# Kernel optimization log

Hardware: AMD Instinct MI355X
Metric: run time of the kernel (lower is better)

The kernel has to match this reference:

```python
import jax, jax.numpy as jnp
import numpy as np

SFREQ = 200.0
PATCH = 60
STRIDE = 30           # patch_size * (1 - overlap)
NPERSEG = min(PATCH // 2, 32)   # = 30
STEP = NPERSEG // 2   # scipy welch default noverlap = nperseg//2
NSEG = (PATCH - NPERSEG) // STEP + 1
NF = NPERSEG // 2 + 1
_w = 0.5 * (1.0 - np.cos(2.0 * np.pi * np.arange(NPERSEG) / NPERSEG))  # periodic hann (scipy default)
HANN = jnp.asarray(_w, jnp.float32)
WIN_NORM = float(SFREQ * np.sum(_w ** 2))  # density scaling
_f = np.arange(NF) * SFREQ / NPERSEG
FREQS = jnp.asarray(_f, jnp.float32)
BANDS = jnp.asarray(np.stack([((_f >= lo) & (_f <= hi)).astype(np.float32)
                              for lo, hi in [(1, 4), (4, 8), (8, 13), (13, 30), (30, 99)]]), jnp.float32)
ONESIDED = jnp.asarray(np.concatenate([[1.0], 2.0 * np.ones(NF - 2), [1.0]]), jnp.float32)


def layer_norm(v, g, b, eps=1e-5):
    mu = v.mean(-1, keepdims=True)
    var = ((v - mu) ** 2).mean(-1, keepdims=True)
    return (v - mu) * jax.lax.rsqrt(var + eps) * g + b


def features(p):
    # p: (B, P, PATCH)
    L = p.shape[-1]
    mx = p.max(-1); mn = p.min(-1); mean = p.mean(-1)
    c = p - mean[..., None]
    m2 = (c ** 2).mean(-1); m3 = (c ** 3).mean(-1); m4 = (c ** 4).mean(-1)
    std = jnp.sqrt(m2)
    peak_loc = jnp.argmax(jnp.abs(p), -1).astype(jnp.float32) / L
    dx = jnp.diff(p, axis=-1)
    zc = jnp.sum(jnp.diff(jnp.sign(p + 1e-10), axis=-1) != 0, axis=-1).astype(jnp.float32) / L
    kurt = m4 / (m2 ** 2) - 3.0   # scipy Fisher, biased
    skew = m3 / (m2 ** 1.5)
    morph = jnp.stack([mx, mn, mx - mn, mean, std, peak_loc,
                       dx.max(-1), dx.min(-1), jnp.abs(dx).mean(-1),
                       zc, (p ** 2).sum(-1), kurt, skew], -1)
    morph = jnp.where(jnp.isfinite(morph), morph, 0.0)
    # Welch PSD (detrend='constant', hann, density, one-sided, mean over segments)
    seg_idx = jnp.arange(NSEG)[:, None] * STEP + jnp.arange(NPERSEG)
    segs = p[..., seg_idx]                             # (B,P,NSEG,NPERSEG)
    segs = (segs - segs.mean(-1, keepdims=True)) * HANN
    X = jnp.fft.rfft(segs, axis=-1)                    # (B,P,NSEG,NF)
    psd = ((X.real ** 2 + X.imag ** 2) / WIN_NORM * ONESIDED).mean(-2)  # (B,P,NF)
    total = psd.sum(-1) + 1e-12
    bandp = jnp.einsum('bpf,kf->bpk', psd, BANDS) / total[..., None]
    peakf = FREQS[jnp.argmax(psd, -1)]
    cs = jnp.cumsum(psd, -1)
    edge = FREQS[jnp.argmax(cs >= 0.95 * total[..., None], -1)]
    pn = psd / total[..., None]
    ent = -jnp.sum(pn * jnp.log2(pn + 1e-12), -1)
    spec = jnp.concatenate([bandp, jnp.stack([peakf, edge, ent, total], -1)], -1)
    spec = jnp.where(jnp.isfinite(spec), spec, 0.0)
    return morph, spec


def setup_inputs() -> dict:
    key = jax.random.key(0)
    ks = jax.random.split(key, 8)
    B, T, E = 1024, 6000, 256
    n_m, n_s = 13, 9
    nf = n_m + n_s
    x = jax.random.normal(ks[0], (B, 1, T), jnp.float32)
    return {
        'x': x,
        'g_m': jnp.ones((n_m,), jnp.float32), 'b_m': jnp.zeros((n_m,), jnp.float32),
        'g_s': jnp.ones((n_s,), jnp.float32), 'b_s': jnp.zeros((n_s,), jnp.float32),
        'W1': jax.random.normal(ks[1], (nf, E // 2), jnp.float32) * 0.05,
        'b1': jnp.zeros((E // 2,), jnp.float32),
        'W2': jax.random.normal(ks[2], (E // 2, E), jnp.float32) * 0.05,
        'b2': jnp.zeros((E,), jnp.float32),
        'g_o': jnp.ones((E,), jnp.float32), 'b_o': jnp.zeros((E,), jnp.float32),
    }


def reference(x, g_m, b_m, g_s, b_s, W1, b1, W2, b2, g_o, b_o):
    B, _, T = x.shape
    n_patches = (T - PATCH) // STRIDE + 1
    idx = jnp.arange(n_patches)[:, None] * STRIDE + jnp.arange(PATCH)
    p = x[:, 0, :][:, idx]                     # (B, n_patches, PATCH)
    morph, spec = features(p)
    combined = jnp.concatenate([layer_norm(morph, g_m, b_m), layer_norm(spec, g_s, b_s)], -1)
    h = jax.nn.gelu(combined @ W1 + b1, approximate=False)  # dropout = identity (eval)
    return layer_norm(h @ W2 + b2, g_o, b_o)   # (B, n_patches, emb_size)
```

## Files before the change

kernel.cpp:

```cpp
#include <hip/hip_runtime.h>
#include <math.h>

#define NPERSEG 30
#define STEPW 15
#define NSEG 3
#define NF 16
#define PATCH 60
#define STRIDE 30
#define NP_ROW 199
#define NBATCH 1024
#define T_LEN 6000
#define NPATCH_TOTAL (NBATCH * NP_ROW)
#define GB 32
#define NBLK_B (NPATCH_TOTAL / GB)

constexpr double TC[30] = {
  1.0,
  0.97814760073380563793,
  0.91354545764260089550,
  0.80901699437494742410,
  0.66913060635885821383,
  0.5,
  0.30901699437494742410,
  0.10452846326765347140,
 -0.10452846326765347140,
 -0.30901699437494742410,
 -0.5,
 -0.66913060635885821383,
 -0.80901699437494742410,
 -0.91354545764260089550,
 -0.97814760073380563793,
 -1.0,
 -0.97814760073380563793,
 -0.91354545764260089550,
 -0.80901699437494742410,
 -0.66913060635885821383,
 -0.5,
 -0.30901699437494742410,
 -0.10452846326765347140,
  0.10452846326765347140,
  0.30901699437494742410,
  0.5,
  0.66913060635885821383,
  0.80901699437494742410,
  0.91354545764260089550,
  0.97814760073380563793,
};
constexpr double TS[30] = {
  0.0,
  0.20791169081775933710,
  0.40673664307580020775,
  0.58778525229247312917,
  0.74314482547739423501,
  0.86602540378443864676,
  0.95105651629515357212,
  0.99452189536827333692,
  0.99452189536827333692,
  0.95105651629515357212,
  0.86602540378443864676,
  0.74314482547739423501,
  0.58778525229247312917,
  0.40673664307580020775,
  0.20791169081775933710,
  0.0,
 -0.20791169081775933710,
 -0.40673664307580020775,
 -0.58778525229247312917,
 -0.74314482547739423501,
 -0.86602540378443864676,
 -0.95105651629515357212,
 -0.99452189536827333692,
 -0.99452189536827333692,
 -0.95105651629515357212,
 -0.86602540378443864676,
 -0.74314482547739423501,
 -0.58778525229247312917,
 -0.40673664307580020775,
 -0.20791169081775933710,
};
constexpr double INV_WN = 1.0 / 2250.0;
constexpr double THIRD  = 1.0 / 3.0;

__device__ __forceinline__ float np_sum30_f32(const float* a) {
    float r[8];
#pragma unroll
    for (int j = 0; j < 8; ++j) r[j] = a[j];
#pragma unroll
    for (int i = 8; i < 24; i += 8)
#pragma unroll
        for (int j = 0; j < 8; ++j) r[j] += a[i + j];
    float res = ((r[0] + r[1]) + (r[2] + r[3])) + ((r[4] + r[5]) + (r[6] + r[7]));
#pragma unroll
    for (int i = 24; i < 30; ++i) res += a[i];
    return res;
}

__device__ __forceinline__ double np_sum16_f64(const double* a) {
    double r[8];
#pragma unroll
    for (int j = 0; j < 8; ++j) r[j] = a[j] + a[8 + j];
    return ((r[0] + r[1]) + (r[2] + r[3])) + ((r[4] + r[5]) + (r[6] + r[7]));
}

__global__ __launch_bounds__(256) void feat_kernel(
    const float* __restrict__ x,
    const float* __restrict__ g_m, const float* __restrict__ b_m,
    const float* __restrict__ g_s, const float* __restrict__ b_s,
    float* __restrict__ out)
{
    __shared__ float xs[T_LEN];

    const int tid = threadIdx.x;
    const int row = blockIdx.x;

    {
        const float4* src = reinterpret_cast<const float4*>(x + (size_t)row * T_LEN);
        float4* dst = reinterpret_cast<float4*>(xs);
        for (int i = tid; i < T_LEN / 4; i += 256) dst[i] = src[i];
    }
    __syncthreads();
    if (tid >= NP_ROW) return;

    const float* pf = xs + tid * STRIDE;
    const int p = row * NP_ROW + tid;
    float* op = out + (size_t)(p >> 5) * (GB * 256) + (size_t)(p & 31) * 22;

    double morph[13];
    {
        const float v0f = pf[0];
        const double v0 = (double)v0f;
        double vmax = v0, vmin = v0, vsum = v0;
        float aval = fabsf(v0f); int amax = 0;
        float sv0 = v0f + 1e-10f;
        int prev = (sv0 > 0.0f) - (sv0 < 0.0f);
        int zc = 0;
        double dmax = 0.0, dmin = 0.0, dabssum = 0.0;
        double vprev = v0;
#pragma unroll
        for (int n = 1; n < PATCH; ++n) {
            const float vf = pf[n];
            const double v = (double)vf;
            vmax = fmax(vmax, v); vmin = fmin(vmin, v); vsum += v;
            const float a = fabsf(vf);
            if (a > aval) { aval = a; amax = n; }
            const float sv = vf + 1e-10f;
            const int sg = (sv > 0.0f) - (sv < 0.0f);
            if (sg != prev) zc++;
            prev = sg;
            const double d = v - vprev;
            if (n == 1) { dmax = d; dmin = d; dabssum = fabs(d); }
            else { dmax = fmax(dmax, d); dmin = fmin(dmin, d); dabssum += fabs(d); }
            vprev = v;
        }
        const double vmean = vsum / 60.0;
        const double dabsmean = dabssum / 59.0;
        const double peak_loc = (double)((float)amax / 60.0f);
        const double zcf = (double)zc / 60.0;

        double s2 = 0.0, s3 = 0.0, s4 = 0.0, ssq = 0.0;
#pragma unroll
        for (int n = 0; n < PATCH; ++n) {
            const double v = (double)pf[n];
            const double c = v - vmean, c2 = c * c;
            s2 += c2; s3 += c2 * c; s4 += c2 * c2;
            ssq += v * v;
        }
        const double m2 = s2 / 60.0, m3 = s3 / 60.0, m4 = s4 / 60.0;
        const double vstd = sqrt(m2);
        const double kurt = m4 / (m2 * m2) - 3.0;
        const double skew = m3 / (m2 * sqrt(m2));

        morph[0] = vmax;  morph[1] = vmin;  morph[2] = vmax - vmin;
        morph[3] = vmean; morph[4] = vstd;  morph[5] = peak_loc;
        morph[6] = dmax;  morph[7] = dmin;  morph[8] = dabsmean;
        morph[9] = zcf;   morph[10] = ssq;  morph[11] = kurt; morph[12] = skew;
#pragma unroll
        for (int i = 0; i < 13; ++i) if (!isfinite(morph[i])) morph[i] = 0.0;
    }
    {
        double mu = 0.0;
#pragma unroll
        for (int i = 0; i < 13; ++i) mu += morph[i];
        mu /= 13.0;
        double var = 0.0;
#pragma unroll
        for (int i = 0; i < 13; ++i) { double d = morph[i] - mu; var += d * d; }
        var /= 13.0;
        const double inv = 1.0 / sqrt(var + 1e-5);
        float fm[13];
#pragma unroll
        for (int i = 0; i < 13; ++i)
            fm[i] = (float)((morph[i] - mu) * inv * (double)g_m[i] + (double)b_m[i]);
#pragma unroll
        for (int i = 0; i < 6; ++i)
            *reinterpret_cast<float2*>(op + 2 * i) = make_float2(fm[2 * i], fm[2 * i + 1]);
        op[12] = fm[12];
    }

    asm volatile("" ::: "memory");

    double psd[NF];
#pragma unroll
    for (int k = 0; k < NF; ++k) psd[k] = 0.0;

#pragma unroll 1
    for (int s = 0; s < NSEG; ++s) {
        float y[NPERSEG];
        {
            float q[NPERSEG];
#pragma unroll
            for (int n = 0; n < NPERSEG; ++n) q[n] = pf[s * STEPW + n];
            const float res = np_sum30_f32(q);
            const float smean = res / 30.0f;
#pragma unroll
            for (int n = 0; n < NPERSEG; ++n) {
                const float hn = (float)(0.5 * (1.0 - TC[n]));
                y[n] = (q[n] - smean) * hn;
            }
        }

        {
            double re[8], im[8];
#pragma unroll
            for (int j = 0; j < 8; ++j) { re[j] = 0.0; im[j] = 0.0; }
#pragma unroll
            for (int m = 0; m < NPERSEG; ++m) {
                const double yd = (double)y[m];
#pragma unroll
                for (int j = 0; j < 8; ++j) {
                    const double tcv = TC[(j * m) % 30];
                    const double tsv = TS[(j * m) % 30];
                    re[j] += yd * tcv;
                    if (tsv != 0.0) im[j] += yd * tsv;
                }
            }
#pragma unroll
            for (int j = 0; j < 8; ++j) {
                double pw = re[j] * re[j] + im[j] * im[j];
                pw *= INV_WN;
                if (j != 0) pw = pw + pw;
                psd[j] += pw;
            }
        }
        {
            double re[8], im[8];
#pragma unroll
            for (int j = 0; j < 8; ++j) { re[j] = 0.0; im[j] = 0.0; }
#pragma unroll
            for (int m = 0; m < NPERSEG; ++m) {
                const double yd = (double)y[m];
#pragma unroll
                for (int j = 0; j < 8; ++j) {
                    const int k = 8 + j;
                    const double tcv = TC[(k * m) % 30];
                    const double tsv = TS[(k * m) % 30];
                    re[j] += yd * tcv;
                    if (tsv != 0.0) im[j] += yd * tsv;
                }
            }
#pragma unroll
            for (int j = 0; j < 8; ++j) {
                double pw = re[j] * re[j] + im[j] * im[j];
                pw *= INV_WN;
                if (j != 7) pw = pw + pw;
                psd[8 + j] += pw;
            }
        }
    }
#pragma unroll
    for (int k = 0; k < NF; ++k) psd[k] = psd[k] * THIRD;

    const double total = np_sum16_f64(psd) + 1e-12;
    const double invt = 1.0 / total;

    const double band1 = psd[1] * invt;
    const double band3 = ((psd[2] + psd[3]) + psd[4]) * invt;
    double b4s = 0.0;
#pragma unroll
    for (int k = 5; k <= 14; ++k) b4s += psd[k];
    const double band4 = b4s * invt;

    int bk = 0; double bpv = psd[0];
#pragma unroll
    for (int k = 1; k < NF; ++k) if (psd[k] > bpv) { bpv = psd[k]; bk = k; }

    const double th = 0.95 * total;
    int ek = 0;
    {
        double acc = 0.0; bool found = false;
#pragma unroll
        for (int k = 0; k < NF; ++k) {
            acc += psd[k];
            if (!found && acc >= th) { ek = k; found = true; }
        }
    }

    double ent = 0.0;
#pragma unroll
    for (int k = 0; k < NF; ++k) {
        const double pn = psd[k] * invt;
        ent -= pn * log2(pn + 1e-12);
    }

    double spec[9];
    spec[0] = 0.0;
    spec[1] = band1;
    spec[2] = 0.0;
    spec[3] = band3;
    spec[4] = band4;
    spec[5] = (double)((float)((double)bk * 200.0 / 30.0));
    spec[6] = (double)((float)((double)ek * 200.0 / 30.0));
    spec[7] = ent;
    spec[8] = total;
#pragma unroll
    for (int i = 0; i < 9; ++i) if (!isfinite(spec[i])) spec[i] = 0.0;

    {
        double mu = 0.0;
#pragma unroll
        for (int i = 0; i < 9; ++i) mu += spec[i];
        mu /= 9.0;
        double var = 0.0;
#pragma unroll
        for (int i = 0; i < 9; ++i) { double d = spec[i] - mu; var += d * d; }
        var /= 9.0;
        const double inv = 1.0 / sqrt(var + 1e-5);
        float fs[9];
#pragma unroll
        for (int i = 0; i < 9; ++i)
            fs[i] = (float)((spec[i] - mu) * inv * (double)g_s[i] + (double)b_s[i]);
        op[13] = fs[0];
#pragma unroll
        for (int i = 0; i < 4; ++i)
            *reinterpret_cast<float2*>(op + 14 + 2 * i) = make_float2(fs[1 + 2 * i], fs[2 + 2 * i]);
    }
}

__global__ __launch_bounds__(256, 4) void mlp_kernel(
    const float* __restrict__ W1, const float* __restrict__ b1,
    const float* __restrict__ W2, const float* __restrict__ b2,
    const float* __restrict__ g_o, const float* __restrict__ b_o,
    float* __restrict__ out)
{
    __shared__ float Fsl[GB * 22];
    __shared__ float Hs[GB][128];

    const int tid = threadIdx.x;
    const size_t base = (size_t)blockIdx.x * (GB * 256);

    if (tid < 176)
        reinterpret_cast<float4*>(Fsl)[tid] =
            *reinterpret_cast<const float4*>(out + base + 4 * (size_t)tid);
    __syncthreads();

    {
        const int hc  = tid & 127;
        const int ppb = tid >> 7;
        float w1c[22];
#pragma unroll
        for (int k = 0; k < 22; ++k) w1c[k] = W1[k * 128 + hc];
        const float b1v = b1[hc];
#pragma unroll
        for (int v = 0; v < 16; ++v) {
            const int pp = ppb + 2 * v;
            float a = b1v;
#pragma unroll
            for (int k = 0; k < 22; ++k) a += Fsl[pp * 22 + k] * w1c[k];
            Hs[pp][hc] = 0.5f * a * (1.0f + erff(a * 0.70710678118654752440f));
        }
    }
    __syncthreads();

    const int lane  = tid & 63;
    const int wv    = tid >> 6;
    const int half  = lane >> 5;
    const int l5    = lane & 31;
    const int ch0   = l5 * 8;
    const int pbase = 8 * wv + 4 * half;

    float4 accA[4], accB[4];
    {
        const float4 b2lo = *reinterpret_cast<const float4*>(b2 + ch0);
        const float4 b2hi = *reinterpret_cast<const float4*>(b2 + ch0 + 4);
#pragma unroll
        for (int pp = 0; pp < 4; ++pp) { accA[pp] = b2lo; accB[pp] = b2hi; }
    }

#pragma unroll 2
    for (int k = 0; k < 128; k += 4) {
        float4 h[4];
#pragma unroll
        for (int pp = 0; pp < 4; ++pp)
            h[pp] = *reinterpret_cast<const float4*>(&Hs[pbase + pp][k]);
        float4 wlo[4], whi[4];
#pragma unroll
        for (int kk = 0; kk < 4; ++kk) {
            wlo[kk] = *reinterpret_cast<const float4*>(&W2[(k + kk) * 256 + ch0]);
            whi[kk] = *reinterpret_cast<const float4*>(&W2[(k + kk) * 256 + ch0 + 4]);
        }
#pragma unroll
        for (int kk = 0; kk < 4; ++kk) {
#pragma unroll
            for (int pp = 0; pp < 4; ++pp) {
                const float hv = (kk == 0) ? h[pp].x : (kk == 1) ? h[pp].y
                               : (kk == 2) ? h[pp].z : h[pp].w;
                accA[pp].x += hv * wlo[kk].x; accA[pp].y += hv * wlo[kk].y;
                accA[pp].z += hv * wlo[kk].z; accA[pp].w += hv * wlo[kk].w;
                accB[pp].x += hv * whi[kk].x; accB[pp].y += hv * whi[kk].y;
                accB[pp].z += hv * whi[kk].z; accB[pp].w += hv * whi[kk].w;
            }
        }
    }

    const float4 golo = *reinterpret_cast<const float4*>(g_o + ch0);
    const float4 gohi = *reinterpret_cast<const float4*>(g_o + ch0 + 4);
    const float4 bolo = *reinterpret_cast<const float4*>(b_o + ch0);
    const float4 bohi = *reinterpret_cast<const float4*>(b_o + ch0 + 4);
#pragma unroll
    for (int pp = 0; pp < 4; ++pp) {
        float s = ((accA[pp].x + accA[pp].y) + (accA[pp].z + accA[pp].w))
                + ((accB[pp].x + accB[pp].y) + (accB[pp].z + accB[pp].w));
        float q = ((accA[pp].x * accA[pp].x + accA[pp].y * accA[pp].y)
                +  (accA[pp].z * accA[pp].z + accA[pp].w * accA[pp].w))
                + ((accB[pp].x * accB[pp].x + accB[pp].y * accB[pp].y)
                +  (accB[pp].z * accB[pp].z + accB[pp].w * accB[pp].w));
        for (int off = 16; off; off >>= 1) {
            s += __shfl_xor(s, off);
            q += __shfl_xor(q, off);
        }
        const float mu  = s * (1.0f / 256.0f);
        const float var = q * (1.0f / 256.0f) - mu * mu;
        const float inv = rsqrtf(var + 1e-5f);
        float4 oA, oB;
        oA.x = (accA[pp].x - mu) * inv * golo.x + bolo.x;
        oA.y = (accA[pp].y - mu) * inv * golo.y + bolo.y;
        oA.z = (accA[pp].z - mu) * inv * golo.z + bolo.z;
        oA.w = (accA[pp].w - mu) * inv * golo.w + bolo.w;
        oB.x = (accB[pp].x - mu) * inv * gohi.x + bohi.x;
        oB.y = (accB[pp].y - mu) * inv * gohi.y + bohi.y;
        oB.z = (accB[pp].z - mu) * inv * gohi.z + bohi.z;
        oB.w = (accB[pp].w - mu) * inv * gohi.w + bohi.w;
        float* orow = out + base + (size_t)(pbase + pp) * 256 + ch0;
        *reinterpret_cast<float4*>(orow)     = oA;
        *reinterpret_cast<float4*>(orow + 4) = oB;
    }
}

extern "C" void kernel_launch(void* const* d_in, const int* in_sizes, int n_in,
                              void* d_out, int out_size, void* d_ws, size_t ws_size,
                              hipStream_t stream) {
    const float* x   = (const float*)d_in[0];
    const float* g_m = (const float*)d_in[1];
    const float* b_m = (const float*)d_in[2];
    const float* g_s = (const float*)d_in[3];
    const float* b_s = (const float*)d_in[4];
    const float* W1  = (const float*)d_in[5];
    const float* b1  = (const float*)d_in[6];
    const float* W2  = (const float*)d_in[7];
    const float* b2  = (const float*)d_in[8];
    const float* g_o = (const float*)d_in[9];
    const float* b_o = (const float*)d_in[10];
    float* out = (float*)d_out;

    feat_kernel<<<NBATCH, 256, 0, stream>>>(x, g_m, b_m, g_s, b_s, out);
    mlp_kernel<<<NBLK_B, 256, 0, stream>>>(W1, b1, W2, b2, g_o, b_o, out);
}
```

Baseline: 481.0 us.

## Fold real-input DFT symmetry and remap MLP second layer to one row per wave

The per-segment DFT now pairs y[m] with y[30-m], using their sum for the cosine terms and their difference for the sine terms. This roughly halves the double-precision multiply-adds in the Welch PSD. The second-layer GEMM in the MLP kernel is remapped so each thread owns 4 output channels across 8 patches, with one full wave covering a 256-wide row and a 64-lane reduction for the layer norm. Launch bounds rise to 8 blocks per CU, which restricts register usage and may cause spilling.

```diff
diff --git a/kernel.cpp b/kernel.cpp
--- a/kernel.cpp
+++ b/kernel.cpp
@@ -218,20 +218,26 @@
                 y[n] = (q[n] - smean) * hn;
             }
         }
+        const double y0d  = (double)y[0];
+        const double y15d = (double)y[15];
 
         {
             double re[8], im[8];
 #pragma unroll
-            for (int j = 0; j < 8; ++j) { re[j] = 0.0; im[j] = 0.0; }
-#pragma unroll
-            for (int m = 0; m < NPERSEG; ++m) {
-                const double yd = (double)y[m];
+            for (int j = 0; j < 8; ++j) {
+                re[j] = (j & 1) ? (y0d - y15d) : (y0d + y15d);
+                im[j] = 0.0;
+            }
+#pragma unroll
+            for (int m = 1; m < 15; ++m) {
+                const double u = (double)y[m] + (double)y[NPERSEG - m];
+                const double v = (double)y[m] - (double)y[NPERSEG - m];
 #pragma unroll
                 for (int j = 0; j < 8; ++j) {
                     const double tcv = TC[(j * m) % 30];
                     const double tsv = TS[(j * m) % 30];
-                    re[j] += yd * tcv;
-                    if (tsv != 0.0) im[j] += yd * tsv;
+                    re[j] += u * tcv;
+                    if (tsv != 0.0) im[j] += v * tsv;
                 }
             }
 #pragma unroll
@@ -245,17 +251,21 @@
         {
             double re[8], im[8];
 #pragma unroll
-            for (int j = 0; j < 8; ++j) { re[j] = 0.0; im[j] = 0.0; }
-#pragma unroll
-            for (int m = 0; m < NPERSEG; ++m) {
-                const double yd = (double)y[m];
+            for (int j = 0; j < 8; ++j) {
+                re[j] = (j & 1) ? (y0d - y15d) : (y0d + y15d);
+                im[j] = 0.0;
+            }
+#pragma unroll
+            for (int m = 1; m < 15; ++m) {
+                const double u = (double)y[m] + (double)y[NPERSEG - m];
+                const double v = (double)y[m] - (double)y[NPERSEG - m];
 #pragma unroll
                 for (int j = 0; j < 8; ++j) {
                     const int k = 8 + j;
                     const double tcv = TC[(k * m) % 30];
                     const double tsv = TS[(k * m) % 30];
-                    re[j] += yd * tcv;
-                    if (tsv != 0.0) im[j] += yd * tsv;
+                    re[j] += u * tcv;
+                    if (tsv != 0.0) im[j] += v * tsv;
                 }
             }
 #pragma unroll
@@ -336,7 +346,7 @@
     }
 }
 
-__global__ __launch_bounds__(256, 4) void mlp_kernel(
+__global__ __launch_bounds__(256, 8) void mlp_kernel(
     const float* __restrict__ W1, const float* __restrict__ b1,
     const float* __restrict__ W2, const float* __restrict__ b2,
     const float* __restrict__ g_o, const float* __restrict__ b_o,
@@ -371,78 +381,56 @@
     }
     __syncthreads();
 
-    const int lane  = tid & 63;
-    const int wv    = tid >> 6;
-    const int half  = lane >> 5;
-    const int l5    = lane & 31;
-    const int ch0   = l5 * 8;
-    const int pbase = 8 * wv + 4 * half;
-
-    float4 accA[4], accB[4];
-    {
-        const float4 b2lo = *reinterpret_cast<const float4*>(b2 + ch0);
-        const float4 b2hi = *reinterpret_cast<const float4*>(b2 + ch0 + 4);
-#pragma unroll
-        for (int pp = 0; pp < 4; ++pp) { accA[pp] = b2lo; accB[pp] = b2hi; }
+    const int cb = tid & 63;
+    const int wv = tid >> 6;
+
+    float4 acc[8];
+    {
+        const float4 b2v = *reinterpret_cast<const float4*>(b2 + 4 * cb);
+#pragma unroll
+        for (int p = 0; p < 8; ++p) acc[p] = b2v;
     }
 
 #pragma unroll 2
     for (int k = 0; k < 128; k += 4) {
-        float4 h[4];
-#pragma unroll
-        for (int pp = 0; pp < 4; ++pp)
-            h[pp] = *reinterpret_cast<const float4*>(&Hs[pbase + pp][k]);
-        float4 wlo[4], whi[4];
-#pragma unroll
-        for (int kk = 0; kk < 4; ++kk) {
-            wlo[kk] = *reinterpret_cast<const float4*>(&W2[(k + kk) * 256 + ch0]);
-            whi[kk] = *reinterpret_cast<const float4*>(&W2[(k + kk) * 256 + ch0 + 4]);
-        }
-#pragma unroll
-        for (int kk = 0; kk < 4; ++kk) {
-#pragma unroll
-            for (int pp = 0; pp < 4; ++pp) {
-                const float hv = (kk == 0) ? h[pp].x : (kk == 1) ? h[pp].y
-                               : (kk == 2) ? h[pp].z : h[pp].w;
-                accA[pp].x += hv * wlo[kk].x; accA[pp].y += hv * wlo[kk].y;
-                accA[pp].z += hv * wlo[kk].z; accA[pp].w += hv * wlo[kk].w;
-                accB[pp].x += hv * whi[kk].x; accB[pp].y += hv * whi[kk].y;
-                accB[pp].z += hv * whi[kk].z; accB[pp].w += hv * whi[kk].w;
-            }
-        }
-    }
-
-    const float4 golo = *reinterpret_cast<const float4*>(g_o + ch0);
-    const float4 gohi = *reinterpret_cast<const float4*>(g_o + ch0 + 4);
-    const float4 bolo = *reinterpret_cast<const float4*>(b_o + ch0);
-    const float4 bohi = *reinterpret_cast<const float4*>(b_o + ch0 + 4);
-#pragma unroll
-    for (int pp = 0; pp < 4; ++pp) {
-        float s = ((accA[pp].x + accA[pp].y) + (accA[pp].z + accA[pp].w))
-                + ((accB[pp].x + accB[pp].y) + (accB[pp].z + accB[pp].w));
-        float q = ((accA[pp].x * accA[pp].x + accA[pp].y * accA[pp].y)
-                +  (accA[pp].z * accA[pp].z + accA[pp].w * accA[pp].w))
-                + ((accB[pp].x * accB[pp].x + accB[pp].y * accB[pp].y)
-                +  (accB[pp].z * accB[pp].z + accB[pp].w * accB[pp].w));
-        for (int off = 16; off; off >>= 1) {
+        float4 w0 = *reinterpret_cast<const float4*>(&W2[(k + 0) * 256 + 4 * cb]);
+        float4 w1 = *reinterpret_cast<const float4*>(&W2[(k + 1) * 256 + 4 * cb]);
+        float4 w2 = *reinterpret_cast<const float4*>(&W2[(k + 2) * 256 + 4 * cb]);
+        float4 w3 = *reinterpret_cast<const float4*>(&W2[(k + 3) * 256 + 4 * cb]);
+#pragma unroll
+        for (int p = 0; p < 8; ++p) {
+            const float4 h = *reinterpret_cast<const float4*>(&Hs[8 * wv + p][k]);
+            acc[p].x += h.x * w0.x; acc[p].y += h.x * w0.y;
+            acc[p].z += h.x * w0.z; acc[p].w += h.x * w0.w;
+            acc[p].x += h.y * w1.x; acc[p].y += h.y * w1.y;
+            acc[p].z += h.y * w1.z; acc[p].w += h.y * w1.w;
+            acc[p].x += h.z * w2.x; acc[p].y += h.z * w2.y;
+            acc[p].z += h.z * w2.z; acc[p].w += h.z * w2.w;
+            acc[p].x += h.w * w3.x; acc[p].y += h.w * w3.y;
+            acc[p].z += h.w * w3.z; acc[p].w += h.w * w3.w;
+        }
+    }
+
+    const float4 go4 = *reinterpret_cast<const float4*>(g_o + 4 * cb);
+    const float4 bo4 = *reinterpret_cast<const float4*>(b_o + 4 * cb);
+#pragma unroll
+    for (int p = 0; p < 8; ++p) {
+        float s = (acc[p].x + acc[p].y) + (acc[p].z + acc[p].w);
+        float q = (acc[p].x * acc[p].x + acc[p].y * acc[p].y)
+                + (acc[p].z * acc[p].z + acc[p].w * acc[p].w);
+        for (int off = 32; off; off >>= 1) {
             s += __shfl_xor(s, off);
             q += __shfl_xor(q, off);
         }
         const float mu  = s * (1.0f / 256.0f);
         const float var = q * (1.0f / 256.0f) - mu * mu;
         const float inv = rsqrtf(var + 1e-5f);
-        float4 oA, oB;
-        oA.x = (accA[pp].x - mu) * inv * golo.x + bolo.x;
-        oA.y = (accA[pp].y - mu) * inv * golo.y + bolo.y;
-        oA.z = (accA[pp].z - mu) * inv * golo.z + bolo.z;
-        oA.w = (accA[pp].w - mu) * inv * golo.w + bolo.w;
-        oB.x = (accB[pp].x - mu) * inv * gohi.x + bohi.x;
-        oB.y = (accB[pp].y - mu) * inv * gohi.y + bohi.y;
-        oB.z = (accB[pp].z - mu) * inv * gohi.z + bohi.z;
-        oB.w = (accB[pp].w - mu) * inv * gohi.w + bohi.w;
-        float* orow = out + base + (size_t)(pbase + pp) * 256 + ch0;
-        *reinterpret_cast<float4*>(orow)     = oA;
-        *reinterpret_cast<float4*>(orow + 4) = oB;
+        float4 o;
+        o.x = (acc[p].x - mu) * inv * go4.x + bo4.x;
+        o.y = (acc[p].y - mu) * inv * go4.y + bo4.y;
+        o.z = (acc[p].z - mu) * inv * go4.z + bo4.z;
+        o.w = (acc[p].w - mu) * inv * go4.w + bo4.w;
+        *reinterpret_cast<float4*>(out + base + (size_t)(8 * wv + p) * 256 + 4 * cb) = o;
     }
 }
 
```

After: 443.7 us. 7.8% less time.
